# Optimization experiments

Measured on AMD Instinct MI355X. Metric: run time of the kernel, lower is better.

## Reference

```python
import jax, jax.numpy as jnp
import numpy as np

D_MODEL = 1024
N_HEADS = 16
D_V = D_MODEL // N_HEADS  # 64; o_proj maps d_model -> d_v (quirk of the source)
B, S = 4, 2048


def setup_inputs() -> dict:
    key = jax.random.key(0)
    ks = jax.random.split(key, 5)
    scale = 1.0 / np.sqrt(D_MODEL)
    return {
        "in_features": jax.random.normal(ks[0], (B, S, D_MODEL), dtype=jnp.float32),
        "Wq": jax.random.normal(ks[1], (D_MODEL, D_MODEL), dtype=jnp.float32) * scale,
        "Wk": jax.random.normal(ks[2], (D_MODEL, D_MODEL), dtype=jnp.float32) * scale,
        "Wv": jax.random.normal(ks[3], (D_MODEL, D_MODEL), dtype=jnp.float32) * scale,
        "Wo": jax.random.normal(ks[4], (D_V, D_MODEL), dtype=jnp.float32) * scale,
    }


def reference(in_features, Wq, Wk, Wv, Wo):
    # Linear(in, out): y = x @ W^T, no bias. NOTE: source never splits heads;
    # attention runs single-head over the full d_model dims.
    Q = jnp.einsum('bsd,ed->bse', in_features, Wq)  # [B,S,D]
    K = jnp.einsum('bsd,ed->bse', in_features, Wk)
    V = jnp.einsum('bsd,ed->bse', in_features, Wv)

    scores = jnp.einsum('bqd,bkd->bqk', Q, K)       # [B,S,S]
    causal = jnp.tril(jnp.ones((S, S), dtype=bool))  # True = keep
    # source applies -inf mask BEFORE scaling (equivalent result)
    scores = jnp.where(causal[None, :, :], scores, -jnp.inf)
    scores = scores / jnp.sqrt(jnp.float32(D_MODEL))  # K.size(-1) == d_model
    attn = jax.nn.softmax(scores, axis=-1)
    ctx = jnp.einsum('bqk,bkd->bqd', attn, V)        # [B,S,D]
    return jnp.einsum('bsd,vd->bsv', ctx, Wo)        # [B,S,D_V]
```

## Files before the change

### kernel.cpp

```cpp
#include <hip/hip_runtime.h>
#include <math.h>

typedef unsigned short u16;
typedef unsigned int u32;
typedef __attribute__((ext_vector_type(8))) short short8;
typedef __attribute__((ext_vector_type(4))) short short4v;
typedef __attribute__((ext_vector_type(4))) float f32x4;

#define BB 4
#define SS 2048
#define DD 1024
#define DV 64
#define NYU 1152
#define BS (BB * SS)
#define SCALE (1.0f / 32.0f)

__device__ __forceinline__ u16 f2bf(float f) {
    u32 u = __builtin_bit_cast(u32, f);
    u32 r = u + 0x7fffu + ((u >> 16) & 1u);
    return (u16)(r >> 16);
}
__device__ __forceinline__ float bf2f(u16 b) {
    return __builtin_bit_cast(float, (u32)b << 16);
}
__device__ __forceinline__ void storeC(float* p, float v) { *p = v; }
__device__ __forceinline__ void storeC(u16* p, float v) { *p = f2bf(v); }

template <int N>
__device__ __forceinline__ void wait_vm() {
    if constexpr (N == 0) asm volatile("s_waitcnt vmcnt(0)" ::: "memory");
    else if constexpr (N == 1) asm volatile("s_waitcnt vmcnt(1)" ::: "memory");
    else if constexpr (N == 2) asm volatile("s_waitcnt vmcnt(2)" ::: "memory");
    else if constexpr (N == 3) asm volatile("s_waitcnt vmcnt(3)" ::: "memory");
    else if constexpr (N == 4) asm volatile("s_waitcnt vmcnt(4)" ::: "memory");
    else if constexpr (N == 6) asm volatile("s_waitcnt vmcnt(6)" ::: "memory");
    else if constexpr (N == 8) asm volatile("s_waitcnt vmcnt(8)" ::: "memory");
}

__global__ __launch_bounds__(256) void prep(const float* __restrict__ x,
                                            const float* __restrict__ Wq,
                                            const float* __restrict__ Wk,
                                            const float* __restrict__ Wo,
                                            const float* __restrict__ Wv,
                                            u16* __restrict__ x16,
                                            u16* __restrict__ Wqt,
                                            u16* __restrict__ Wkt,
                                            float* __restrict__ wpart,
                                            float* __restrict__ out,
                                            float* __restrict__ Lacc) {
    __shared__ float smem[64 * 128];
    const int b = blockIdx.x;
    const int tid = threadIdx.x;
    if (b < 64) {
        const int bb = b;
        const int echunk = (bb & 7) * 128;
        const int kc = bb >> 3, kbase = kc * 128;
        for (int idx = tid; idx < 64 * 128; idx += 256)
            smem[idx] = Wo[(size_t)(idx >> 7) * DD + kbase + (idx & 127)];
        __syncthreads();
        const int eo = echunk + (tid & 31) * 4;
        const int ob = (tid >> 5) * 8;
        float acc[8][4] = {};
        for (int k = 0; k < 128; ++k) {
            f32x4 wv = *(const f32x4*)&Wv[(size_t)(kbase + k) * DD + eo];
#pragma unroll
            for (int oi = 0; oi < 8; ++oi) {
                float s = smem[(ob + oi) * 128 + k];
                acc[oi][0] += s * wv.x; acc[oi][1] += s * wv.y;
                acc[oi][2] += s * wv.z; acc[oi][3] += s * wv.w;
            }
        }
#pragma unroll
        for (int oi = 0; oi < 8; ++oi)
            *(f32x4*)&wpart[((size_t)kc * 64 + ob + oi) * DD + eo] =
                (f32x4){acc[oi][0], acc[oi][1], acc[oi][2], acc[oi][3]};
    } else if (b < 576) {
        const int bb = b - 64;
        const float* src = (bb >> 8) ? Wk : Wq;
        u16* dst = (bb >> 8) ? Wkt : Wqt;
        const int rem = bb & 255;
        const int e0 = (rem >> 4) * 64, d0 = (rem & 15) * 64;
        u16* t = (u16*)smem;
        const int g = tid >> 6, lane = tid & 63;
        for (int r = g; r < 64; r += 4)
            t[r * 72 + lane] = f2bf(src[(size_t)(e0 + r) * DD + d0 + lane]);
        __syncthreads();
        for (int r = g; r < 64; r += 4)
            dst[(size_t)(d0 + r) * DD + e0 + lane] = t[lane * 72 + r];
    } else if (b < 8768) {
        int i = (b - 576) * 256 + tid;
        f32x4 v = ((const f32x4*)x)[i];
        short4v o;
        o.x = (short)f2bf(v.x); o.y = (short)f2bf(v.y);
        o.z = (short)f2bf(v.z); o.w = (short)f2bf(v.w);
        ((short4v*)x16)[i] = o;
    } else if (b < 9280) {
        int i = (b - 8768) * 256 + tid;
        ((f32x4*)out)[i] = (f32x4){0.f, 0.f, 0.f, 0.f};
    } else {
        int i = (b - 9280) * 256 + tid;
        ((f32x4*)Lacc)[i] = (f32x4){0.f, 0.f, 0.f, 0.f};
    }
}

__global__ __launch_bounds__(256) void reduce_all(const float* __restrict__ Gpart,
                                                  const float* __restrict__ wpart,
                                                  u16* __restrict__ Wall2) {
    const int bx = blockIdx.x;
    const int e0 = threadIdx.x * 4;
    f32x4 s = (f32x4){0.f, 0.f, 0.f, 0.f};
    if (bx < 1024) {
#pragma unroll
        for (int kc = 0; kc < 4; ++kc)
            s += *(const f32x4*)&Gpart[(size_t)kc * DD * DD + (size_t)bx * DD + e0];
    } else {
#pragma unroll
        for (int kc = 0; kc < 8; ++kc)
            s += *(const f32x4*)&wpart[((size_t)kc * 64 + bx - 1024) * DD + e0];
    }
    short4v ov;
    ov.x = (short)f2bf(s.x); ov.y = (short)f2bf(s.y);
    ov.z = (short)f2bf(s.z); ov.w = (short)f2bf(s.w);
    *(short4v*)&Wall2[(size_t)bx * DD + e0] = ov;
}

template <int TM, int TN, int WM, int WN, typename OutT, int MODE>
__global__ __launch_bounds__(WM * WN * 64) void gemm_nt_mfma(
    const u16* __restrict__ A, const u16* __restrict__ B, OutT* __restrict__ C,
    int lda, int ldb, int ldc, int K, long sA, long sB, long sC,
    u16* __restrict__ Utp) {
    constexpr int NW = WM * WN;
    constexpr int CA = TM / 16;
    constexpr int CB = TN / 16;
    constexpr int RT = TM / WM;
    constexpr int CT = TN / WN;
    constexpr int AI = RT / 16;
    constexpr int AJ = CT / 16;
    constexpr int LPT = CA / NW + CB / NW;

    const int z = blockIdx.z;
    A += (size_t)z * sA;
    B += (size_t)z * sB;
    C += (size_t)z * sC;
    int m0, n0;
    if constexpr (MODE == 3) {
        const int b = blockIdx.x;
        const int r = b & 7, q = b >> 3;
        constexpr int RPX = 8192 / TM / 8;
        m0 = (r * RPX + q / 9) * TM;
        n0 = (q % 9) * TN;
    } else {
        m0 = blockIdx.y * TM;
        n0 = blockIdx.x * TN;
    }

    __shared__ u16 As[3][TM * 32];
    __shared__ u16 Bs[3][TN * 32];

    const int tid = threadIdx.x;
    const int w = tid >> 6, lane = tid & 63;
    const int wm = w / WN, wn = w % WN;
    const int lrow = lane >> 2;
    const int lcolsw = (((lane & 3) ^ ((lrow >> 1) & 3)) << 3);
    const int m16 = lane & 15;
    const int rdo = (((lane >> 4) ^ ((m16 >> 1) & 3)) << 3);

    f32x4 acc[AI][AJ];
#pragma unroll
    for (int i = 0; i < AI; ++i)
#pragma unroll
        for (int j = 0; j < AJ; ++j) acc[i][j] = (f32x4){0.f, 0.f, 0.f, 0.f};

    auto stage = [&](int t, int bufi) {
        const int k0 = t * 32;
        for (int c = w; c < CA; c += NW) {
            const u16* g = A + (size_t)(m0 + c * 16 + lrow) * lda + k0 + lcolsw;
            __builtin_amdgcn_global_load_lds(
                (const __attribute__((address_space(1))) void*)g,
                (__attribute__((address_space(3))) void*)(&As[bufi][c * 512]), 16, 0, 0);
        }
        for (int c = w; c < CB; c += NW) {
            const u16* g = B + (size_t)(n0 + c * 16 + lrow) * ldb + k0 + lcolsw;
            __builtin_amdgcn_global_load_lds(
                (const __attribute__((address_space(1))) void*)g,
                (__attribute__((address_space(3))) void*)(&Bs[bufi][c * 512]), 16, 0, 0);
        }
    };

    const int nk = K >> 5;
    stage(0, 0);
    if (nk > 1) { stage(1, 1); wait_vm<LPT>(); } else { wait_vm<0>(); }
    __syncthreads();

    int rb = 0, sb = 2;
    for (int t = 0; t < nk; ++t) {
        if (t + 2 < nk) stage(t + 2, sb);

        short8 a[AI], b[AJ];
#pragma unroll
        for (int i = 0; i < AI; ++i)
            a[i] = *(const short8*)&As[rb][(wm * RT + i * 16 + m16) * 32 + rdo];
#pragma unroll
        for (int j = 0; j < AJ; ++j)
            b[j] = *(const short8*)&Bs[rb][(wn * CT + j * 16 + m16) * 32 + rdo];
#pragma unroll
        for (int i = 0; i < AI; ++i)
#pragma unroll
            for (int j = 0; j < AJ; ++j)
                acc[i][j] = __builtin_amdgcn_mfma_f32_16x16x32_bf16(a[i], b[j], acc[i][j], 0, 0, 0);

        if (t + 2 < nk) { wait_vm<LPT>(); __syncthreads(); }
        else if (t + 1 < nk) { wait_vm<0>(); __syncthreads(); }
        rb = (rb == 2) ? 0 : rb + 1;
        sb = (sb == 2) ? 0 : sb + 1;
    }

    const int crow0 = m0 + wm * RT + (lane >> 4) * 4;
    const int ccol0 = n0 + wn * CT + m16;
#pragma unroll
    for (int i = 0; i < AI; ++i)
#pragma unroll
        for (int j = 0; j < AJ; ++j)
#pragma unroll
            for (int r = 0; r < 4; ++r) {
                const float v = acc[i][j][r];
                storeC(&C[(size_t)(crow0 + i * 16 + r) * ldc + ccol0 + j * 16], v);
                if constexpr (MODE == 3) {
                    if (n0 == 1024 && wn == 0)
                        Utp[(size_t)(ccol0 + j * 16 - 1024) * BS + crow0 + i * 16 + r] = f2bf(v);
                }
            }
}

__global__ __launch_bounds__(256) void scores_pv(const u16* __restrict__ YU,
                                                 const u16* __restrict__ x16,
                                                 const u16* __restrict__ Ut,
                                                 float* __restrict__ out,
                                                 float* __restrict__ Lacc) {
    const int b = blockIdx.x;
    const int r8 = b & 7;
    const int z = r8 >> 1;
    const int t = 2 * (b >> 3) + (r8 & 1);
    int y = (int)((sqrtf(8.f * t + 1.f) - 1.f) * 0.5f);
    while ((y + 1) * (y + 2) / 2 <= t) ++y;
    while (y * (y + 1) / 2 > t) --y;
    const int m0 = y * 128;
    const int n0 = (t - y * (y + 1) / 2) * 128;

    const u16* A = YU + (size_t)z * SS * NYU;
    const u16* B = x16 + (size_t)z * SS * DD;

    __shared__ union ShU {
        struct { u16 As[3][128 * 32]; u16 Bs[3][128 * 32]; } s;
        u16 Ps[128 * 136];
    } sh;

    const int tid = threadIdx.x;
    const int w = tid >> 6, lane = tid & 63;
    const int wm = w >> 1, wn = w & 1;
    const int lrow = lane >> 2;
    const int lcolsw = (((lane & 3) ^ ((lrow >> 1) & 3)) << 3);
    const int m16 = lane & 15;
    const int kh = (lane >> 4) * 8;
    const int rdo = (((lane >> 4) ^ ((m16 >> 1) & 3)) << 3);

    f32x4 acc[4][4];
#pragma unroll
    for (int i = 0; i < 4; ++i)
#pragma unroll
        for (int j = 0; j < 4; ++j) acc[i][j] = (f32x4){0.f, 0.f, 0.f, 0.f};

    auto stage = [&](int tt, int bufi) {
        const int k0 = tt * 32;
        for (int c = w; c < 8; c += 4) {
            const u16* g = A + (size_t)(m0 + c * 16 + lrow) * NYU + k0 + lcolsw;
            __builtin_amdgcn_global_load_lds(
                (const __attribute__((address_space(1))) void*)g,
                (__attribute__((address_space(3))) void*)(&sh.s.As[bufi][c * 512]), 16, 0, 0);
        }
        for (int c = w; c < 8; c += 4) {
            const u16* g = B + (size_t)(n0 + c * 16 + lrow) * DD + k0 + lcolsw;
            __builtin_amdgcn_global_load_lds(
                (const __attribute__((address_space(1))) void*)g,
                (__attribute__((address_space(3))) void*)(&sh.s.Bs[bufi][c * 512]), 16, 0, 0);
        }
    };

    stage(0, 0);
    stage(1, 1);
    wait_vm<4>();
    __syncthreads();

    int rb = 0, sb = 2;
    for (int tt = 0; tt < 32; ++tt) {
        if (tt + 2 < 32) stage(tt + 2, sb);

        short8 a[4], bb[4];
#pragma unroll
        for (int i = 0; i < 4; ++i)
            a[i] = *(const short8*)&sh.s.As[rb][(wm * 64 + i * 16 + m16) * 32 + rdo];
#pragma unroll
        for (int j = 0; j < 4; ++j)
            bb[j] = *(const short8*)&sh.s.Bs[rb][(wn * 64 + j * 16 + m16) * 32 + rdo];
#pragma unroll
        for (int i = 0; i < 4; ++i)
#pragma unroll
            for (int j = 0; j < 4; ++j)
                acc[i][j] = __builtin_amdgcn_mfma_f32_16x16x32_bf16(a[i], bb[j], acc[i][j], 0, 0, 0);

        if (tt + 2 < 32) { wait_vm<4>(); __syncthreads(); }
        else if (tt + 1 < 32) { wait_vm<0>(); __syncthreads(); }
        rb = (rb == 2) ? 0 : rb + 1;
        sb = (sb == 2) ? 0 : sb + 1;
    }
    __syncthreads();

    const int rl0 = wm * 64 + (lane >> 4) * 4;
    const int cl0 = wn * 64 + m16;
#pragma unroll
    for (int i = 0; i < 4; ++i)
#pragma unroll
        for (int j = 0; j < 4; ++j)
#pragma unroll
            for (int r = 0; r < 4; ++r) {
                const int rl = rl0 + i * 16 + r;
                const int cl = cl0 + j * 16;
                float p = __expf(acc[i][j][r] * SCALE);
                sh.Ps[rl * 136 + cl] = (n0 + cl <= m0 + rl) ? f2bf(p) : (u16)0;
            }
    __syncthreads();

    short8 ones8;
#pragma unroll
    for (int e = 0; e < 8; ++e) ones8[e] = (short)0x3F80;

    const u16* Utz = Ut + (size_t)z * SS + n0;
    f32x4 accO[2][4], accL[2];
#pragma unroll
    for (int i = 0; i < 2; ++i) {
        accL[i] = (f32x4){0.f, 0.f, 0.f, 0.f};
#pragma unroll
        for (int j = 0; j < 4; ++j) accO[i][j] = (f32x4){0.f, 0.f, 0.f, 0.f};
    }
#pragma unroll
    for (int ks = 0; ks < 4; ++ks) {
        const int k0 = ks * 32;
        short8 a[2], bb[4];
#pragma unroll
        for (int i = 0; i < 2; ++i)
            a[i] = *(const short8*)&sh.Ps[(w * 32 + i * 16 + m16) * 136 + k0 + kh];
#pragma unroll
        for (int j = 0; j < 4; ++j)
            bb[j] = *(const short8*)&Utz[(size_t)(j * 16 + m16) * BS + k0 + kh];
#pragma unroll
        for (int i = 0; i < 2; ++i) {
#pragma unroll
            for (int j = 0; j < 4; ++j)
                accO[i][j] = __builtin_amdgcn_mfma_f32_16x16x32_bf16(a[i], bb[j], accO[i][j], 0, 0, 0);
            accL[i] = __builtin_amdgcn_mfma_f32_16x16x32_bf16(a[i], ones8, accL[i], 0, 0, 0);
        }
    }

    float* Oz = out + (size_t)z * SS * DV;
    float* Lz = Lacc + (size_t)z * SS;
    const int wrow = m0 + w * 32 + (lane >> 4) * 4;
#pragma unroll
    for (int i = 0; i < 2; ++i) {
#pragma unroll
        for (int j = 0; j < 4; ++j)
#pragma unroll
            for (int r = 0; r < 4; ++r)
                atomicAdd(&Oz[(size_t)(wrow + i * 16 + r) * DV + j * 16 + m16],
                          accO[i][j][r]);
        if (m16 == 0)
#pragma unroll
            for (int r = 0; r < 4; ++r)
                atomicAdd(&Lz[wrow + i * 16 + r], accL[i][r]);
    }
}

__global__ __launch_bounds__(256) void normalize(float* __restrict__ out,
                                                 const float* __restrict__ Lacc) {
    int i = blockIdx.x * 256 + threadIdx.x;
    f32x4 v = ((f32x4*)out)[i];
    const float inv = 1.f / Lacc[(i * 4) >> 6];
    v.x *= inv; v.y *= inv; v.z *= inv; v.w *= inv;
    ((f32x4*)out)[i] = v;
}

extern "C" void kernel_launch(void* const* d_in, const int* in_sizes, int n_in,
                              void* d_out, int out_size, void* d_ws, size_t ws_size,
                              hipStream_t stream) {
    const float* x  = (const float*)d_in[0];
    const float* Wq = (const float*)d_in[1];
    const float* Wk = (const float*)d_in[2];
    const float* Wv = (const float*)d_in[3];
    const float* Wo = (const float*)d_in[4];
    float* out = (float*)d_out;

    u16* x16   = (u16*)d_ws;
    u16* Wqt16 = x16 + (size_t)BB * SS * DD;
    u16* Wkt16 = Wqt16 + (size_t)DD * DD;
    u16* Wall2 = Wkt16 + (size_t)DD * DD;
    u16* YU    = Wall2 + (size_t)NYU * DD;
    u16* Ut    = YU + (size_t)BB * SS * NYU;
    float* wpart = (float*)(Ut + (size_t)DV * BS);
    float* Lacc  = wpart + (size_t)8 * 64 * DD;
    float* Gpart = (float*)YU;

    prep<<<dim3(9288), 256, 0, stream>>>(x, Wq, Wk, Wo, Wv, x16, Wqt16, Wkt16,
                                         wpart, out, Lacc);

    gemm_nt_mfma<64, 64, 2, 2, float, 0><<<dim3(16, 16, 4), 256, 0, stream>>>(
        Wkt16, Wqt16, Gpart, DD, DD, DD, 256, 256, 256, (long)DD * DD, nullptr);

    reduce_all<<<dim3(1088), 256, 0, stream>>>(Gpart, wpart, Wall2);

    gemm_nt_mfma<128, 128, 2, 2, u16, 3><<<dim3(576), 256, 0, stream>>>(
        x16, Wall2, YU, DD, DD, NYU, DD, 0, 0, 0, Ut);

    scores_pv<<<dim3(544), 256, 0, stream>>>(YU, x16, Ut, out, Lacc);

    normalize<<<dim3(out_size / 4 / 256), 256, 0, stream>>>(out, Lacc);
}
```

Before: 193.1 us.

## Switch GEMM K-loop to BK=64 double buffering with new LDS swizzle and setprio

Both the generic NT GEMM and the attention score kernel move from a 3-stage, BK=32 pipeline to a 2-stage, BK=64 pipeline. The loads use a new 8-row by 64-column XOR swizzle, and each tile is consumed in two 32-wide MFMA sub-steps. This halves the number of barriers and K iterations and raises wave priority around the MFMA block with s_setprio. In exchange, prefetch depth drops to one tile with a full vmcnt(0) wait each iteration, which may expose memory latency. LDS per block also grows, which could lower occupancy.

```diff
diff --git a/kernel.cpp b/kernel.cpp
--- a/kernel.cpp
+++ b/kernel.cpp
@@ -25,17 +25,6 @@
 }
 __device__ __forceinline__ void storeC(float* p, float v) { *p = v; }
 __device__ __forceinline__ void storeC(u16* p, float v) { *p = f2bf(v); }
-
-template <int N>
-__device__ __forceinline__ void wait_vm() {
-    if constexpr (N == 0) asm volatile("s_waitcnt vmcnt(0)" ::: "memory");
-    else if constexpr (N == 1) asm volatile("s_waitcnt vmcnt(1)" ::: "memory");
-    else if constexpr (N == 2) asm volatile("s_waitcnt vmcnt(2)" ::: "memory");
-    else if constexpr (N == 3) asm volatile("s_waitcnt vmcnt(3)" ::: "memory");
-    else if constexpr (N == 4) asm volatile("s_waitcnt vmcnt(4)" ::: "memory");
-    else if constexpr (N == 6) asm volatile("s_waitcnt vmcnt(6)" ::: "memory");
-    else if constexpr (N == 8) asm volatile("s_waitcnt vmcnt(8)" ::: "memory");
-}
 
 __global__ __launch_bounds__(256) void prep(const float* __restrict__ x,
                                             const float* __restrict__ Wq,
@@ -130,13 +119,12 @@
     int lda, int ldb, int ldc, int K, long sA, long sB, long sC,
     u16* __restrict__ Utp) {
     constexpr int NW = WM * WN;
-    constexpr int CA = TM / 16;
-    constexpr int CB = TN / 16;
+    constexpr int LA = TM / 8;
+    constexpr int LB = TN / 8;
     constexpr int RT = TM / WM;
     constexpr int CT = TN / WN;
     constexpr int AI = RT / 16;
     constexpr int AJ = CT / 16;
-    constexpr int LPT = CA / NW + CB / NW;
 
     const int z = blockIdx.z;
     A += (size_t)z * sA;
@@ -154,16 +142,16 @@
         n0 = blockIdx.x * TN;
     }
 
-    __shared__ u16 As[3][TM * 32];
-    __shared__ u16 Bs[3][TN * 32];
+    __shared__ u16 As[2][TM * 64];
+    __shared__ u16 Bs[2][TN * 64];
 
     const int tid = threadIdx.x;
     const int w = tid >> 6, lane = tid & 63;
     const int wm = w / WN, wn = w % WN;
-    const int lrow = lane >> 2;
-    const int lcolsw = (((lane & 3) ^ ((lrow >> 1) & 3)) << 3);
+    const int rsub = lane >> 3;
+    const int gsw = (((lane & 7) ^ rsub) << 3);
     const int m16 = lane & 15;
-    const int rdo = (((lane >> 4) ^ ((m16 >> 1) & 3)) << 3);
+    const int g0 = (((lane >> 4) ^ (m16 & 7)) << 3);
 
     f32x4 acc[AI][AJ];
 #pragma unroll
@@ -172,47 +160,54 @@
         for (int j = 0; j < AJ; ++j) acc[i][j] = (f32x4){0.f, 0.f, 0.f, 0.f};
 
     auto stage = [&](int t, int bufi) {
-        const int k0 = t * 32;
-        for (int c = w; c < CA; c += NW) {
-            const u16* g = A + (size_t)(m0 + c * 16 + lrow) * lda + k0 + lcolsw;
+        const int k0 = t * 64;
+        for (int c = w; c < LA; c += NW) {
+            const u16* g = A + (size_t)(m0 + c * 8 + rsub) * lda + k0 + gsw;
             __builtin_amdgcn_global_load_lds(
                 (const __attribute__((address_space(1))) void*)g,
                 (__attribute__((address_space(3))) void*)(&As[bufi][c * 512]), 16, 0, 0);
         }
-        for (int c = w; c < CB; c += NW) {
-            const u16* g = B + (size_t)(n0 + c * 16 + lrow) * ldb + k0 + lcolsw;
+        for (int c = w; c < LB; c += NW) {
+            const u16* g = B + (size_t)(n0 + c * 8 + rsub) * ldb + k0 + gsw;
             __builtin_amdgcn_global_load_lds(
                 (const __attribute__((address_space(1))) void*)g,
                 (__attribute__((address_space(3))) void*)(&Bs[bufi][c * 512]), 16, 0, 0);
         }
     };
 
-    const int nk = K >> 5;
+    const int nk = K >> 6;
     stage(0, 0);
-    if (nk > 1) { stage(1, 1); wait_vm<LPT>(); } else { wait_vm<0>(); }
+    asm volatile("s_waitcnt vmcnt(0)" ::: "memory");
     __syncthreads();
 
-    int rb = 0, sb = 2;
+    int cur = 0;
     for (int t = 0; t < nk; ++t) {
-        if (t + 2 < nk) stage(t + 2, sb);
-
-        short8 a[AI], b[AJ];
-#pragma unroll
-        for (int i = 0; i < AI; ++i)
-            a[i] = *(const short8*)&As[rb][(wm * RT + i * 16 + m16) * 32 + rdo];
-#pragma unroll
-        for (int j = 0; j < AJ; ++j)
-            b[j] = *(const short8*)&Bs[rb][(wn * CT + j * 16 + m16) * 32 + rdo];
-#pragma unroll
-        for (int i = 0; i < AI; ++i)
+        if (t + 1 < nk) stage(t + 1, cur ^ 1);
+
+        __builtin_amdgcn_s_setprio(1);
+#pragma unroll
+        for (int ks = 0; ks < 2; ++ks) {
+            const int off = g0 ^ (ks << 5);
+            short8 a[AI], b[AJ];
+#pragma unroll
+            for (int i = 0; i < AI; ++i)
+                a[i] = *(const short8*)&As[cur][(wm * RT + i * 16 + m16) * 64 + off];
 #pragma unroll
             for (int j = 0; j < AJ; ++j)
-                acc[i][j] = __builtin_amdgcn_mfma_f32_16x16x32_bf16(a[i], b[j], acc[i][j], 0, 0, 0);
-
-        if (t + 2 < nk) { wait_vm<LPT>(); __syncthreads(); }
-        else if (t + 1 < nk) { wait_vm<0>(); __syncthreads(); }
-        rb = (rb == 2) ? 0 : rb + 1;
-        sb = (sb == 2) ? 0 : sb + 1;
+                b[j] = *(const short8*)&Bs[cur][(wn * CT + j * 16 + m16) * 64 + off];
+#pragma unroll
+            for (int i = 0; i < AI; ++i)
+#pragma unroll
+                for (int j = 0; j < AJ; ++j)
+                    acc[i][j] = __builtin_amdgcn_mfma_f32_16x16x32_bf16(a[i], b[j], acc[i][j], 0, 0, 0);
+        }
+        __builtin_amdgcn_s_setprio(0);
+
+        if (t + 1 < nk) {
+            asm volatile("s_waitcnt vmcnt(0)" ::: "memory");
+            __syncthreads();
+        }
+        cur ^= 1;
     }
 
     const int crow0 = m0 + wm * RT + (lane >> 4) * 4;
@@ -251,18 +246,18 @@
     const u16* B = x16 + (size_t)z * SS * DD;
 
     __shared__ union ShU {
-        struct { u16 As[3][128 * 32]; u16 Bs[3][128 * 32]; } s;
+        struct { u16 As[2][128 * 64]; u16 Bs[2][128 * 64]; } s;
         u16 Ps[128 * 136];
     } sh;
 
     const int tid = threadIdx.x;
     const int w = tid >> 6, lane = tid & 63;
     const int wm = w >> 1, wn = w & 1;
-    const int lrow = lane >> 2;
-    const int lcolsw = (((lane & 3) ^ ((lrow >> 1) & 3)) << 3);
+    const int rsub = lane >> 3;
+    const int gsw = (((lane & 7) ^ rsub) << 3);
     const int m16 = lane & 15;
     const int kh = (lane >> 4) * 8;
-    const int rdo = (((lane >> 4) ^ ((m16 >> 1) & 3)) << 3);
+    const int g0 = (((lane >> 4) ^ (m16 & 7)) << 3);
 
     f32x4 acc[4][4];
 #pragma unroll
@@ -271,15 +266,15 @@
         for (int j = 0; j < 4; ++j) acc[i][j] = (f32x4){0.f, 0.f, 0.f, 0.f};
 
     auto stage = [&](int tt, int bufi) {
-        const int k0 = tt * 32;
-        for (int c = w; c < 8; c += 4) {
-            const u16* g = A + (size_t)(m0 + c * 16 + lrow) * NYU + k0 + lcolsw;
+        const int k0 = tt * 64;
+        for (int c = w; c < 16; c += 4) {
+            const u16* g = A + (size_t)(m0 + c * 8 + rsub) * NYU + k0 + gsw;
             __builtin_amdgcn_global_load_lds(
                 (const __attribute__((address_space(1))) void*)g,
                 (__attribute__((address_space(3))) void*)(&sh.s.As[bufi][c * 512]), 16, 0, 0);
         }
-        for (int c = w; c < 8; c += 4) {
-            const u16* g = B + (size_t)(n0 + c * 16 + lrow) * DD + k0 + lcolsw;
+        for (int c = w; c < 16; c += 4) {
+            const u16* g = B + (size_t)(n0 + c * 8 + rsub) * DD + k0 + gsw;
             __builtin_amdgcn_global_load_lds(
                 (const __attribute__((address_space(1))) void*)g,
                 (__attribute__((address_space(3))) void*)(&sh.s.Bs[bufi][c * 512]), 16, 0, 0);
@@ -287,31 +282,37 @@
     };
 
     stage(0, 0);
-    stage(1, 1);
-    wait_vm<4>();
+    asm volatile("s_waitcnt vmcnt(0)" ::: "memory");
     __syncthreads();
 
-    int rb = 0, sb = 2;
-    for (int tt = 0; tt < 32; ++tt) {
-        if (tt + 2 < 32) stage(tt + 2, sb);
-
-        short8 a[4], bb[4];
-#pragma unroll
-        for (int i = 0; i < 4; ++i)
-            a[i] = *(const short8*)&sh.s.As[rb][(wm * 64 + i * 16 + m16) * 32 + rdo];
-#pragma unroll
-        for (int j = 0; j < 4; ++j)
-            bb[j] = *(const short8*)&sh.s.Bs[rb][(wn * 64 + j * 16 + m16) * 32 + rdo];
-#pragma unroll
-        for (int i = 0; i < 4; ++i)
+    int cur = 0;
+    for (int tt = 0; tt < 16; ++tt) {
+        if (tt + 1 < 16) stage(tt + 1, cur ^ 1);
+
+        __builtin_amdgcn_s_setprio(1);
+#pragma unroll
+        for (int ks = 0; ks < 2; ++ks) {
+            const int off = g0 ^ (ks << 5);
+            short8 a[4], bb[4];
+#pragma unroll
+            for (int i = 0; i < 4; ++i)
+                a[i] = *(const short8*)&sh.s.As[cur][(wm * 64 + i * 16 + m16) * 64 + off];
 #pragma unroll
             for (int j = 0; j < 4; ++j)
-                acc[i][j] = __builtin_amdgcn_mfma_f32_16x16x32_bf16(a[i], bb[j], acc[i][j], 0, 0, 0);
-
-        if (tt + 2 < 32) { wait_vm<4>(); __syncthreads(); }
-        else if (tt + 1 < 32) { wait_vm<0>(); __syncthreads(); }
-        rb = (rb == 2) ? 0 : rb + 1;
-        sb = (sb == 2) ? 0 : sb + 1;
+                bb[j] = *(const short8*)&sh.s.Bs[cur][(wn * 64 + j * 16 + m16) * 64 + off];
+#pragma unroll
+            for (int i = 0; i < 4; ++i)
+#pragma unroll
+                for (int j = 0; j < 4; ++j)
+                    acc[i][j] = __builtin_amdgcn_mfma_f32_16x16x32_bf16(a[i], bb[j], acc[i][j], 0, 0, 0);
+        }
+        __builtin_amdgcn_s_setprio(0);
+
+        if (tt + 1 < 16) {
+            asm volatile("s_waitcnt vmcnt(0)" ::: "memory");
+            __syncthreads();
+        }
+        cur ^= 1;
     }
     __syncthreads();
 
```

After: 212.1 us. 1.1x slower.

## Shrink GEMM and scores tiles to 64x128 with two-stage double buffering

Applied to the files above, without the earlier changes.

The projection GEMM and the fused scores/PV kernel move from 128x128 tiles with 4 waves and a 3-stage LDS pipeline to 64x128 tiles with 2 waves and a 2-stage double buffer. The grid doubles and a new triangular index mapping covers 64-row query tiles. The aim is more blocks and lower LDS use per block so occupancy and load balance improve across the CUs. In exchange, each stage waits for all loads to finish (vmcnt 0) before computing, so less memory latency is hidden, and the smaller tiles reuse each loaded operand less.

```diff
diff --git a/kernel.cpp b/kernel.cpp
--- a/kernel.cpp
+++ b/kernel.cpp
@@ -25,17 +25,6 @@
 }
 __device__ __forceinline__ void storeC(float* p, float v) { *p = v; }
 __device__ __forceinline__ void storeC(u16* p, float v) { *p = f2bf(v); }
-
-template <int N>
-__device__ __forceinline__ void wait_vm() {
-    if constexpr (N == 0) asm volatile("s_waitcnt vmcnt(0)" ::: "memory");
-    else if constexpr (N == 1) asm volatile("s_waitcnt vmcnt(1)" ::: "memory");
-    else if constexpr (N == 2) asm volatile("s_waitcnt vmcnt(2)" ::: "memory");
-    else if constexpr (N == 3) asm volatile("s_waitcnt vmcnt(3)" ::: "memory");
-    else if constexpr (N == 4) asm volatile("s_waitcnt vmcnt(4)" ::: "memory");
-    else if constexpr (N == 6) asm volatile("s_waitcnt vmcnt(6)" ::: "memory");
-    else if constexpr (N == 8) asm volatile("s_waitcnt vmcnt(8)" ::: "memory");
-}
 
 __global__ __launch_bounds__(256) void prep(const float* __restrict__ x,
                                             const float* __restrict__ Wq,
@@ -136,7 +125,6 @@
     constexpr int CT = TN / WN;
     constexpr int AI = RT / 16;
     constexpr int AJ = CT / 16;
-    constexpr int LPT = CA / NW + CB / NW;
 
     const int z = blockIdx.z;
     A += (size_t)z * sA;
@@ -147,15 +135,16 @@
         const int b = blockIdx.x;
         const int r = b & 7, q = b >> 3;
         constexpr int RPX = 8192 / TM / 8;
-        m0 = (r * RPX + q / 9) * TM;
-        n0 = (q % 9) * TN;
+        constexpr int NP = 1152 / TN;
+        m0 = (r * RPX + q / NP) * TM;
+        n0 = (q % NP) * TN;
     } else {
         m0 = blockIdx.y * TM;
         n0 = blockIdx.x * TN;
     }
 
-    __shared__ u16 As[3][TM * 32];
-    __shared__ u16 Bs[3][TN * 32];
+    __shared__ u16 As[2][TM * 32];
+    __shared__ u16 Bs[2][TN * 32];
 
     const int tid = threadIdx.x;
     const int w = tid >> 6, lane = tid & 63;
@@ -189,30 +178,31 @@
 
     const int nk = K >> 5;
     stage(0, 0);
-    if (nk > 1) { stage(1, 1); wait_vm<LPT>(); } else { wait_vm<0>(); }
+    asm volatile("s_waitcnt vmcnt(0)" ::: "memory");
     __syncthreads();
 
-    int rb = 0, sb = 2;
+    int cur = 0;
     for (int t = 0; t < nk; ++t) {
-        if (t + 2 < nk) stage(t + 2, sb);
+        if (t + 1 < nk) stage(t + 1, cur ^ 1);
 
         short8 a[AI], b[AJ];
 #pragma unroll
         for (int i = 0; i < AI; ++i)
-            a[i] = *(const short8*)&As[rb][(wm * RT + i * 16 + m16) * 32 + rdo];
+            a[i] = *(const short8*)&As[cur][(wm * RT + i * 16 + m16) * 32 + rdo];
 #pragma unroll
         for (int j = 0; j < AJ; ++j)
-            b[j] = *(const short8*)&Bs[rb][(wn * CT + j * 16 + m16) * 32 + rdo];
+            b[j] = *(const short8*)&Bs[cur][(wn * CT + j * 16 + m16) * 32 + rdo];
 #pragma unroll
         for (int i = 0; i < AI; ++i)
 #pragma unroll
             for (int j = 0; j < AJ; ++j)
                 acc[i][j] = __builtin_amdgcn_mfma_f32_16x16x32_bf16(a[i], b[j], acc[i][j], 0, 0, 0);
 
-        if (t + 2 < nk) { wait_vm<LPT>(); __syncthreads(); }
-        else if (t + 1 < nk) { wait_vm<0>(); __syncthreads(); }
-        rb = (rb == 2) ? 0 : rb + 1;
-        sb = (sb == 2) ? 0 : sb + 1;
+        if (t + 1 < nk) {
+            asm volatile("s_waitcnt vmcnt(0)" ::: "memory");
+            __syncthreads();
+        }
+        cur ^= 1;
     }
 
     const int crow0 = m0 + wm * RT + (lane >> 4) * 4;
@@ -226,13 +216,13 @@
                 const float v = acc[i][j][r];
                 storeC(&C[(size_t)(crow0 + i * 16 + r) * ldc + ccol0 + j * 16], v);
                 if constexpr (MODE == 3) {
-                    if (n0 == 1024 && wn == 0)
+                    if (n0 + wn * CT == 1024)
                         Utp[(size_t)(ccol0 + j * 16 - 1024) * BS + crow0 + i * 16 + r] = f2bf(v);
                 }
             }
 }
 
-__global__ __launch_bounds__(256) void scores_pv(const u16* __restrict__ YU,
+__global__ __launch_bounds__(128) void scores_pv(const u16* __restrict__ YU,
                                                  const u16* __restrict__ x16,
                                                  const u16* __restrict__ Ut,
                                                  float* __restrict__ out,
@@ -241,23 +231,24 @@
     const int r8 = b & 7;
     const int z = r8 >> 1;
     const int t = 2 * (b >> 3) + (r8 & 1);
-    int y = (int)((sqrtf(8.f * t + 1.f) - 1.f) * 0.5f);
-    while ((y + 1) * (y + 2) / 2 <= t) ++y;
-    while (y * (y + 1) / 2 > t) --y;
-    const int m0 = y * 128;
-    const int n0 = (t - y * (y + 1) / 2) * 128;
+    auto cum = [](int yy) { int h = yy >> 1; return (yy & 1) ? (h + 1) * (h + 1) : h * (h + 1); };
+    int y = (int)(2.0f * sqrtf((float)t + 0.25f));
+    if (y > 31) y = 31;
+    while (y < 31 && cum(y + 1) <= t) ++y;
+    while (y > 0 && cum(y) > t) --y;
+    const int m0 = y * 64;
+    const int n0 = (t - cum(y)) * 128;
 
     const u16* A = YU + (size_t)z * SS * NYU;
     const u16* B = x16 + (size_t)z * SS * DD;
 
     __shared__ union ShU {
-        struct { u16 As[3][128 * 32]; u16 Bs[3][128 * 32]; } s;
-        u16 Ps[128 * 136];
+        struct { u16 As[2][64 * 32]; u16 Bs[2][128 * 32]; } s;
+        u16 Ps[64 * 136];
     } sh;
 
     const int tid = threadIdx.x;
     const int w = tid >> 6, lane = tid & 63;
-    const int wm = w >> 1, wn = w & 1;
     const int lrow = lane >> 2;
     const int lcolsw = (((lane & 3) ^ ((lrow >> 1) & 3)) << 3);
     const int m16 = lane & 15;
@@ -272,13 +263,13 @@
 
     auto stage = [&](int tt, int bufi) {
         const int k0 = tt * 32;
-        for (int c = w; c < 8; c += 4) {
+        for (int c = w; c < 4; c += 2) {
             const u16* g = A + (size_t)(m0 + c * 16 + lrow) * NYU + k0 + lcolsw;
             __builtin_amdgcn_global_load_lds(
                 (const __attribute__((address_space(1))) void*)g,
                 (__attribute__((address_space(3))) void*)(&sh.s.As[bufi][c * 512]), 16, 0, 0);
         }
-        for (int c = w; c < 8; c += 4) {
+        for (int c = w; c < 8; c += 2) {
             const u16* g = B + (size_t)(n0 + c * 16 + lrow) * DD + k0 + lcolsw;
             __builtin_amdgcn_global_load_lds(
                 (const __attribute__((address_space(1))) void*)g,
@@ -287,36 +278,36 @@
     };
 
     stage(0, 0);
-    stage(1, 1);
-    wait_vm<4>();
+    asm volatile("s_waitcnt vmcnt(0)" ::: "memory");
     __syncthreads();
 
-    int rb = 0, sb = 2;
+    int cur = 0;
     for (int tt = 0; tt < 32; ++tt) {
-        if (tt + 2 < 32) stage(tt + 2, sb);
+        if (tt + 1 < 32) stage(tt + 1, cur ^ 1);
 
         short8 a[4], bb[4];
 #pragma unroll
         for (int i = 0; i < 4; ++i)
-            a[i] = *(const short8*)&sh.s.As[rb][(wm * 64 + i * 16 + m16) * 32 + rdo];
+            a[i] = *(const short8*)&sh.s.As[cur][(i * 16 + m16) * 32 + rdo];
 #pragma unroll
         for (int j = 0; j < 4; ++j)
-            bb[j] = *(const short8*)&sh.s.Bs[rb][(wn * 64 + j * 16 + m16) * 32 + rdo];
+            bb[j] = *(const short8*)&sh.s.Bs[cur][(w * 64 + j * 16 + m16) * 32 + rdo];
 #pragma unroll
         for (int i = 0; i < 4; ++i)
 #pragma unroll
             for (int j = 0; j < 4; ++j)
                 acc[i][j] = __builtin_amdgcn_mfma_f32_16x16x32_bf16(a[i], bb[j], acc[i][j], 0, 0, 0);
 
-        if (tt + 2 < 32) { wait_vm<4>(); __syncthreads(); }
-        else if (tt + 1 < 32) { wait_vm<0>(); __syncthreads(); }
-        rb = (rb == 2) ? 0 : rb + 1;
-        sb = (sb == 2) ? 0 : sb + 1;
+        if (tt + 1 < 32) {
+            asm volatile("s_waitcnt vmcnt(0)" ::: "memory");
+            __syncthreads();
+        }
+        cur ^= 1;
     }
     __syncthreads();
 
-    const int rl0 = wm * 64 + (lane >> 4) * 4;
-    const int cl0 = wn * 64 + m16;
+    const int rl0 = (lane >> 4) * 4;
+    const int cl0 = w * 64 + m16;
 #pragma unroll
     for (int i = 0; i < 4; ++i)
 #pragma unroll
@@ -416,10 +407,10 @@
 
     reduce_all<<<dim3(1088), 256, 0, stream>>>(Gpart, wpart, Wall2);
 
-    gemm_nt_mfma<128, 128, 2, 2, u16, 3><<<dim3(576), 256, 0, stream>>>(
+    gemm_nt_mfma<64, 128, 1, 2, u16, 3><<<dim3(1152), 128, 0, stream>>>(
         x16, Wall2, YU, DD, DD, NYU, DD, 0, 0, 0, Ut);
 
-    scores_pv<<<dim3(544), 256, 0, stream>>>(YU, x16, Ut, out, Lacc);
+    scores_pv<<<dim3(1088), 128, 0, stream>>>(YU, x16, Ut, out, Lacc);
 
     normalize<<<dim3(out_size / 4 / 256), 256, 0, stream>>>(out, Lacc);
 }
```

New measurement: 200.0 us. +3.6%, slower.

## Replace LDS-staged GEMM mainloops with direct global-to-register double-buffered loads

Applied to the files above, without the earlier changes.

Both the generic NT GEMM and the fused scores/PV kernel stop staging A/B tiles through triple-buffered LDS via global_load_lds with barriers. Each wave now loads its MFMA fragments straight from global memory into registers, alternating between two register sets. This removes LDS traffic and block-wide syncs, but tiles shared across waves are fetched redundantly from global/L2 and each load is a 16-byte strided access. The MODE 3 tile mapping and Ut-write condition are generalized for other TN values.

```diff
diff --git a/kernel.cpp b/kernel.cpp
--- a/kernel.cpp
+++ b/kernel.cpp
@@ -25,17 +25,6 @@
 }
 __device__ __forceinline__ void storeC(float* p, float v) { *p = v; }
 __device__ __forceinline__ void storeC(u16* p, float v) { *p = f2bf(v); }
-
-template <int N>
-__device__ __forceinline__ void wait_vm() {
-    if constexpr (N == 0) asm volatile("s_waitcnt vmcnt(0)" ::: "memory");
-    else if constexpr (N == 1) asm volatile("s_waitcnt vmcnt(1)" ::: "memory");
-    else if constexpr (N == 2) asm volatile("s_waitcnt vmcnt(2)" ::: "memory");
-    else if constexpr (N == 3) asm volatile("s_waitcnt vmcnt(3)" ::: "memory");
-    else if constexpr (N == 4) asm volatile("s_waitcnt vmcnt(4)" ::: "memory");
-    else if constexpr (N == 6) asm volatile("s_waitcnt vmcnt(6)" ::: "memory");
-    else if constexpr (N == 8) asm volatile("s_waitcnt vmcnt(8)" ::: "memory");
-}
 
 __global__ __launch_bounds__(256) void prep(const float* __restrict__ x,
                                             const float* __restrict__ Wq,
@@ -129,14 +118,10 @@
     const u16* __restrict__ A, const u16* __restrict__ B, OutT* __restrict__ C,
     int lda, int ldb, int ldc, int K, long sA, long sB, long sC,
     u16* __restrict__ Utp) {
-    constexpr int NW = WM * WN;
-    constexpr int CA = TM / 16;
-    constexpr int CB = TN / 16;
     constexpr int RT = TM / WM;
     constexpr int CT = TN / WN;
     constexpr int AI = RT / 16;
     constexpr int AJ = CT / 16;
-    constexpr int LPT = CA / NW + CB / NW;
 
     const int z = blockIdx.z;
     A += (size_t)z * sA;
@@ -147,23 +132,22 @@
         const int b = blockIdx.x;
         const int r = b & 7, q = b >> 3;
         constexpr int RPX = 8192 / TM / 8;
-        m0 = (r * RPX + q / 9) * TM;
-        n0 = (q % 9) * TN;
+        constexpr int NP = 1152 / TN;
+        m0 = (r * RPX + q / NP) * TM;
+        n0 = (q % NP) * TN;
     } else {
         m0 = blockIdx.y * TM;
         n0 = blockIdx.x * TN;
     }
 
-    __shared__ u16 As[3][TM * 32];
-    __shared__ u16 Bs[3][TN * 32];
-
     const int tid = threadIdx.x;
     const int w = tid >> 6, lane = tid & 63;
     const int wm = w / WN, wn = w % WN;
-    const int lrow = lane >> 2;
-    const int lcolsw = (((lane & 3) ^ ((lrow >> 1) & 3)) << 3);
     const int m16 = lane & 15;
-    const int rdo = (((lane >> 4) ^ ((m16 >> 1) & 3)) << 3);
+    const int kh = (lane >> 4) * 8;
+
+    const u16* aptr = A + (size_t)(m0 + wm * RT + m16) * lda + kh;
+    const u16* bptr = B + (size_t)(n0 + wn * CT + m16) * ldb + kh;
 
     f32x4 acc[AI][AJ];
 #pragma unroll
@@ -171,48 +155,31 @@
 #pragma unroll
         for (int j = 0; j < AJ; ++j) acc[i][j] = (f32x4){0.f, 0.f, 0.f, 0.f};
 
-    auto stage = [&](int t, int bufi) {
-        const int k0 = t * 32;
-        for (int c = w; c < CA; c += NW) {
-            const u16* g = A + (size_t)(m0 + c * 16 + lrow) * lda + k0 + lcolsw;
-            __builtin_amdgcn_global_load_lds(
-                (const __attribute__((address_space(1))) void*)g,
-                (__attribute__((address_space(3))) void*)(&As[bufi][c * 512]), 16, 0, 0);
-        }
-        for (int c = w; c < CB; c += NW) {
-            const u16* g = B + (size_t)(n0 + c * 16 + lrow) * ldb + k0 + lcolsw;
-            __builtin_amdgcn_global_load_lds(
-                (const __attribute__((address_space(1))) void*)g,
-                (__attribute__((address_space(3))) void*)(&Bs[bufi][c * 512]), 16, 0, 0);
-        }
+    auto loadf = [&](short8 (&af)[AI], short8 (&bf)[AJ], int t) {
+        const int ko = t * 32;
+#pragma unroll
+        for (int i = 0; i < AI; ++i)
+            af[i] = *(const short8*)(aptr + (size_t)i * 16 * lda + ko);
+#pragma unroll
+        for (int j = 0; j < AJ; ++j)
+            bf[j] = *(const short8*)(bptr + (size_t)j * 16 * ldb + ko);
     };
+    auto mfma_all = [&](short8 (&af)[AI], short8 (&bf)[AJ]) {
+#pragma unroll
+        for (int i = 0; i < AI; ++i)
+#pragma unroll
+            for (int j = 0; j < AJ; ++j)
+                acc[i][j] = __builtin_amdgcn_mfma_f32_16x16x32_bf16(af[i], bf[j], acc[i][j], 0, 0, 0);
+    };
 
     const int nk = K >> 5;
-    stage(0, 0);
-    if (nk > 1) { stage(1, 1); wait_vm<LPT>(); } else { wait_vm<0>(); }
-    __syncthreads();
-
-    int rb = 0, sb = 2;
-    for (int t = 0; t < nk; ++t) {
-        if (t + 2 < nk) stage(t + 2, sb);
-
-        short8 a[AI], b[AJ];
-#pragma unroll
-        for (int i = 0; i < AI; ++i)
-            a[i] = *(const short8*)&As[rb][(wm * RT + i * 16 + m16) * 32 + rdo];
-#pragma unroll
-        for (int j = 0; j < AJ; ++j)
-            b[j] = *(const short8*)&Bs[rb][(wn * CT + j * 16 + m16) * 32 + rdo];
-#pragma unroll
-        for (int i = 0; i < AI; ++i)
-#pragma unroll
-            for (int j = 0; j < AJ; ++j)
-                acc[i][j] = __builtin_amdgcn_mfma_f32_16x16x32_bf16(a[i], b[j], acc[i][j], 0, 0, 0);
-
-        if (t + 2 < nk) { wait_vm<LPT>(); __syncthreads(); }
-        else if (t + 1 < nk) { wait_vm<0>(); __syncthreads(); }
-        rb = (rb == 2) ? 0 : rb + 1;
-        sb = (sb == 2) ? 0 : sb + 1;
+    short8 aA[AI], bA[AJ], aB[AI], bB[AJ];
+    loadf(aA, bA, 0);
+    for (int t = 0; t < nk; t += 2) {
+        if (t + 1 < nk) loadf(aB, bB, t + 1);
+        mfma_all(aA, bA);
+        if (t + 2 < nk) loadf(aA, bA, t + 2);
+        if (t + 1 < nk) mfma_all(aB, bB);
     }
 
     const int crow0 = m0 + wm * RT + (lane >> 4) * 4;
@@ -226,7 +193,7 @@
                 const float v = acc[i][j][r];
                 storeC(&C[(size_t)(crow0 + i * 16 + r) * ldc + ccol0 + j * 16], v);
                 if constexpr (MODE == 3) {
-                    if (n0 == 1024 && wn == 0)
+                    if (n0 + wn * CT == 1024)
                         Utp[(size_t)(ccol0 + j * 16 - 1024) * BS + crow0 + i * 16 + r] = f2bf(v);
                 }
             }
@@ -250,19 +217,16 @@
     const u16* A = YU + (size_t)z * SS * NYU;
     const u16* B = x16 + (size_t)z * SS * DD;
 
-    __shared__ union ShU {
-        struct { u16 As[3][128 * 32]; u16 Bs[3][128 * 32]; } s;
-        u16 Ps[128 * 136];
-    } sh;
+    __shared__ u16 Ps[128 * 136];
 
     const int tid = threadIdx.x;
     const int w = tid >> 6, lane = tid & 63;
     const int wm = w >> 1, wn = w & 1;
-    const int lrow = lane >> 2;
-    const int lcolsw = (((lane & 3) ^ ((lrow >> 1) & 3)) << 3);
     const int m16 = lane & 15;
     const int kh = (lane >> 4) * 8;
-    const int rdo = (((lane >> 4) ^ ((m16 >> 1) & 3)) << 3);
+
+    const u16* aptr = A + (size_t)(m0 + wm * 64 + m16) * NYU + kh;
+    const u16* bptr = B + (size_t)(n0 + wn * 64 + m16) * DD + kh;
 
     f32x4 acc[4][4];
 #pragma unroll
@@ -270,50 +234,31 @@
 #pragma unroll
         for (int j = 0; j < 4; ++j) acc[i][j] = (f32x4){0.f, 0.f, 0.f, 0.f};
 
-    auto stage = [&](int tt, int bufi) {
-        const int k0 = tt * 32;
-        for (int c = w; c < 8; c += 4) {
-            const u16* g = A + (size_t)(m0 + c * 16 + lrow) * NYU + k0 + lcolsw;
-            __builtin_amdgcn_global_load_lds(
-                (const __attribute__((address_space(1))) void*)g,
-                (__attribute__((address_space(3))) void*)(&sh.s.As[bufi][c * 512]), 16, 0, 0);
-        }
-        for (int c = w; c < 8; c += 4) {
-            const u16* g = B + (size_t)(n0 + c * 16 + lrow) * DD + k0 + lcolsw;
-            __builtin_amdgcn_global_load_lds(
-                (const __attribute__((address_space(1))) void*)g,
-                (__attribute__((address_space(3))) void*)(&sh.s.Bs[bufi][c * 512]), 16, 0, 0);
-        }
+    auto loadf = [&](short8 (&af)[4], short8 (&bf)[4], int tt) {
+        const int ko = tt * 32;
+#pragma unroll
+        for (int i = 0; i < 4; ++i)
+            af[i] = *(const short8*)(aptr + (size_t)i * 16 * NYU + ko);
+#pragma unroll
+        for (int j = 0; j < 4; ++j)
+            bf[j] = *(const short8*)(bptr + (size_t)j * 16 * DD + ko);
     };
-
-    stage(0, 0);
-    stage(1, 1);
-    wait_vm<4>();
-    __syncthreads();
-
-    int rb = 0, sb = 2;
-    for (int tt = 0; tt < 32; ++tt) {
-        if (tt + 2 < 32) stage(tt + 2, sb);
-
-        short8 a[4], bb[4];
+    auto mfma_all = [&](short8 (&af)[4], short8 (&bf)[4]) {
 #pragma unroll
         for (int i = 0; i < 4; ++i)
-            a[i] = *(const short8*)&sh.s.As[rb][(wm * 64 + i * 16 + m16) * 32 + rdo];
-#pragma unroll
-        for (int j = 0; j < 4; ++j)
-            bb[j] = *(const short8*)&sh.s.Bs[rb][(wn * 64 + j * 16 + m16) * 32 + rdo];
-#pragma unroll
-        for (int i = 0; i < 4; ++i)
 #pragma unroll
             for (int j = 0; j < 4; ++j)
-                acc[i][j] = __builtin_amdgcn_mfma_f32_16x16x32_bf16(a[i], bb[j], acc[i][j], 0, 0, 0);
-
-        if (tt + 2 < 32) { wait_vm<4>(); __syncthreads(); }
-        else if (tt + 1 < 32) { wait_vm<0>(); __syncthreads(); }
-        rb = (rb == 2) ? 0 : rb + 1;
-        sb = (sb == 2) ? 0 : sb + 1;
-    }
-    __syncthreads();
+                acc[i][j] = __builtin_amdgcn_mfma_f32_16x16x32_bf16(af[i], bf[j], acc[i][j], 0, 0, 0);
+    };
+
+    short8 aA[4], bA[4], aB[4], bB[4];
+    loadf(aA, bA, 0);
+    for (int tt = 0; tt < 32; tt += 2) {
+        if (tt + 1 < 32) loadf(aB, bB, tt + 1);
+        mfma_all(aA, bA);
+        if (tt + 2 < 32) loadf(aA, bA, tt + 2);
+        if (tt + 1 < 32) mfma_all(aB, bB);
+    }
 
     const int rl0 = wm * 64 + (lane >> 4) * 4;
     const int cl0 = wn * 64 + m16;
@@ -326,7 +271,7 @@
                 const int rl = rl0 + i * 16 + r;
                 const int cl = cl0 + j * 16;
                 float p = __expf(acc[i][j][r] * SCALE);
-                sh.Ps[rl * 136 + cl] = (n0 + cl <= m0 + rl) ? f2bf(p) : (u16)0;
+                Ps[rl * 136 + cl] = (n0 + cl <= m0 + rl) ? f2bf(p) : (u16)0;
             }
     __syncthreads();
 
@@ -348,7 +293,7 @@
         short8 a[2], bb[4];
 #pragma unroll
         for (int i = 0; i < 2; ++i)
-            a[i] = *(const short8*)&sh.Ps[(w * 32 + i * 16 + m16) * 136 + k0 + kh];
+            a[i] = *(const short8*)&Ps[(w * 32 + i * 16 + m16) * 136 + k0 + kh];
 #pragma unroll
         for (int j = 0; j < 4; ++j)
             bb[j] = *(const short8*)&Utz[(size_t)(j * 16 + m16) * BS + k0 + kh];
```

New measurement: 320.8 us. 66.1% more time.
